# Kernel tuning notes

Measured on AMD Instinct MI355X. Metric: run time of the kernel, lower is better.

The kernel has to match this reference:

```python
import jax, jax.numpy as jnp
import numpy as np

IN_FEATURES = 512
OUT_FEATURES = 10
NEURONS_STRUCTURES = [64, 128, 256, 512]
REPETITIONS = 5
NUM_ACTIVATIONS = 4  # relu, tanh, sigmoid, gelu (exact erf, matching torch nn.GELU)
NUM_MODELS = NUM_ACTIVATIONS * REPETITIONS * len(NEURONS_STRUCTURES)  # 80
TOTAL_HIDDEN = sum(NEURONS_STRUCTURES) * REPETITIONS * NUM_ACTIVATIONS  # 19200
BATCH = 1024


def _build_neuron_model_id():
    # Mirrors ParallelMLPs.__init__ construction order:
    # for act -> for rep -> for structure: assign consecutive model ids
    ids = []
    m = 0
    for _act in range(NUM_ACTIVATIONS):
        for _rep in range(REPETITIONS):
            for n in NEURONS_STRUCTURES:
                ids += [m] * n
                m += 1
    return np.asarray(ids, dtype=np.int32)


def setup_inputs() -> dict:
    key = jax.random.key(0)
    k1, k2, k3, k4, k5 = jax.random.split(key, 5)
    x = jax.random.normal(k1, (BATCH, IN_FEATURES), dtype=jnp.float32)
    hidden_w = jax.random.normal(k2, (TOTAL_HIDDEN, IN_FEATURES), dtype=jnp.float32) * 0.05
    hidden_b = jax.random.normal(k3, (TOTAL_HIDDEN,), dtype=jnp.float32) * 0.05
    out_w = jax.random.normal(k4, (OUT_FEATURES, TOTAL_HIDDEN), dtype=jnp.float32) * 0.05
    out_b = jax.random.normal(k5, (NUM_MODELS, OUT_FEATURES), dtype=jnp.float32) * 0.05
    neuron_model_id = jnp.asarray(_build_neuron_model_id())
    return {"x": x, "hidden_w": hidden_w, "hidden_b": hidden_b,
            "out_w": out_w, "out_b": out_b, "neuron_model_id": neuron_model_id}


def reference(x, hidden_w, hidden_b, out_w, out_b, neuron_model_id):
    # Shared hidden linear: [B, H]
    h = x @ hidden_w.T + hidden_b
    # Per-block activations on equal contiguous chunks of the hidden dim
    split = TOTAL_HIDDEN // NUM_ACTIVATIONS
    acts = [jax.nn.relu, jnp.tanh, jax.nn.sigmoid,
            lambda t: jax.nn.gelu(t, approximate=False)]
    a = jnp.concatenate(
        [f(h[:, i * split:(i + 1) * split]) for i, f in enumerate(acts)], axis=1)
    # Ragged grouped out-projection: contrib[h, b, o] = a[b, h] * out_w[o, h]
    contrib = a.T[:, :, None] * out_w.T[:, None, :]  # [H, B, O]
    grouped = jax.ops.segment_sum(contrib, neuron_model_id,
                                  num_segments=NUM_MODELS)  # [M, B, O]
    return jnp.transpose(grouped, (1, 0, 2)) + out_b[None, :, :]  # [B, M, O]
```

## Files before the change

kernel.cpp:

```cpp
#include <hip/hip_runtime.h>
#include <hip/hip_bf16.h>
#include <cstdint>
#include <cstddef>


typedef unsigned short u16;
typedef unsigned int u32;
typedef __bf16 bf16x8 __attribute__((ext_vector_type(8)));
typedef float f32x4 __attribute__((ext_vector_type(4)));

__device__ __forceinline__ u16 f2bf(float f) {
  u32 u = __builtin_bit_cast(u32, f);
  u += 0x7fffu + ((u >> 16) & 1u);
  return (u16)(u >> 16);
}
__device__ __forceinline__ float bf2f(u16 s) {
  u32 u = ((u32)s) << 16;
  return __builtin_bit_cast(float, u);
}

__device__ __forceinline__ void async16(void* l, const void* g) {
  __builtin_amdgcn_global_load_lds(
      (__attribute__((address_space(1))) void*)(void*)g,
      (__attribute__((address_space(3))) void*)l, 16, 0, 0);
}

__global__ __launch_bounds__(256) void cvt_kernel(
    const float4* __restrict__ xs, uint2* __restrict__ xd, int nx4,
    const float4* __restrict__ ws, uint2* __restrict__ wd, int nw4) {
  int i = blockIdx.x * blockDim.x + threadIdx.x;
  if (i >= nx4 + nw4) return;
  const float4* s; uint2* d; int j;
  if (i < nx4) { s = xs; d = xd; j = i; }
  else         { s = ws; d = wd; j = i - nx4; }
  float4 f = s[j];
  uint2 o;
  o.x = (u32)f2bf(f.x) | ((u32)f2bf(f.y) << 16);
  o.y = (u32)f2bf(f.z) | ((u32)f2bf(f.w) << 16);
  d[j] = o;
}

__global__ __launch_bounds__(256, 2) void gemm_act_kernel(
    const u16* __restrict__ A,
    const u16* __restrict__ Bw,
    const float* __restrict__ hbias,
    u16* __restrict__ aout) {
  __shared__ char lds[65536];
  const int t = threadIdx.x;
  const int lane = t & 63;
  const int w = t >> 6;
  const int bx = blockIdx.x % 150;
  const int by = blockIdx.x / 150;
  const int row0 = by * 128;
  const int col0 = bx * 128;
  const int wr = w >> 1, wc = w & 1;

  f32x4 acc[4][4];
#pragma unroll
  for (int m = 0; m < 4; ++m)
#pragma unroll
    for (int n = 0; n < 4; ++n)
#pragma unroll
      for (int r = 0; r < 4; ++r) acc[m][n][r] = 0.f;

  const int srow = t >> 3;
  const int sc8 = t & 7;

  auto stage = [&](int buf, int kt) {
    const int k0 = kt * 64;
#pragma unroll
    for (int i = 0; i < 4; ++i) {
      int row = i * 32 + srow;
      int c8 = sc8 ^ (row & 7);
      const u16* gA = A + (size_t)(row0 + row) * 512 + k0 + c8 * 8;
      const u16* gB = Bw + (size_t)(col0 + row) * 512 + k0 + c8 * 8;
      char* lA = lds + buf * 16384 + i * 4096 + w * 1024;
      char* lB = lds + 32768 + buf * 16384 + i * 4096 + w * 1024;
      async16(lA, gA);
      async16(lB, gB);
    }
  };

  auto compute = [&](int buf) {
    const char* baseA = lds + buf * 16384;
    const char* baseB = lds + 32768 + buf * 16384;
    const int il = lane & 15;
    const int kb0 = (lane >> 4) * 16;
#pragma unroll
    for (int ks = 0; ks < 2; ++ks) {
      bf16x8 av[4], bv[4];
#pragma unroll
      for (int m = 0; m < 4; ++m) {
        int row = wr * 64 + m * 16 + il;
        int off = row * 128 + ((ks * 64 + kb0) ^ ((row & 7) << 4));
        av[m] = *(const bf16x8*)(baseA + off);
      }
#pragma unroll
      for (int n = 0; n < 4; ++n) {
        int row = wc * 64 + n * 16 + il;
        int off = row * 128 + ((ks * 64 + kb0) ^ ((row & 7) << 4));
        bv[n] = *(const bf16x8*)(baseB + off);
      }
#pragma unroll
      for (int m = 0; m < 4; ++m)
#pragma unroll
        for (int n = 0; n < 4; ++n)
          acc[m][n] = __builtin_amdgcn_mfma_f32_16x16x32_bf16(av[m], bv[n],
                                                              acc[m][n], 0, 0, 0);
    }
  };

  stage(0, 0);
  __syncthreads();
#pragma unroll 2
  for (int kt = 0; kt < 8; ++kt) {
    int cur = kt & 1;
    if (kt < 7) stage(cur ^ 1, kt + 1);
    compute(cur);
    __syncthreads();
  }

  const int il = lane & 15;
  const int q = lane >> 4;
#pragma unroll
  for (int n = 0; n < 4; ++n) {
    int gcol = col0 + wc * 64 + n * 16 + il;
    int act = gcol / 4800;
    float bias = hbias[gcol];
#pragma unroll
    for (int m = 0; m < 4; ++m) {
      int growb = row0 + wr * 64 + m * 16 + q * 4;
#pragma unroll
      for (int r = 0; r < 4; ++r) {
        float v = acc[m][n][r] + bias;
        float o;
        if (act == 0)      o = fmaxf(v, 0.f);
        else if (act == 1) o = tanhf(v);
        else if (act == 2) o = 1.f / (1.f + __expf(-v));
        else               o = 0.5f * v * (1.f + erff(v * 0.70710678118f));
        aout[(size_t)(growb + r) * 19200 + gcol] = f2bf(o);
      }
    }
  }
}

__global__ __launch_bounds__(256) void layer2_kernel(
    const u16* __restrict__ a,
    const float* __restrict__ ow,
    const float* __restrict__ ob,
    float* __restrict__ out) {
  const int t = threadIdx.x;
  const int wid = blockIdx.x * 4 + (t >> 6);
  const int lane = t & 63;
  const int m = wid >> 8;
  const int btile = wid & 255;
  const int g = lane >> 4;
  const int il = lane & 15;
  const int b = btile * 4 + g;
  const int s = m & 3;
  const int r5 = (m >> 2) % 5;
  const int act = m / 20;
  const int start = act * 4800 + r5 * 960 + 64 * ((1 << s) - 1);
  const int len = 64 << s;

  const u16* arow = a + (size_t)b * 19200 + start;
  float acc[10];
#pragma unroll
  for (int o = 0; o < 10; ++o) acc[o] = 0.f;

  for (int j = il; j < len; j += 16) {
    float av = bf2f(arow[j]);
    int col = start + j;
#pragma unroll
    for (int o = 0; o < 10; ++o)
      acc[o] = fmaf(av, ow[o * 19200 + col], acc[o]);
  }
#pragma unroll
  for (int o = 0; o < 10; ++o) {
    float v = acc[o];
    v += __shfl_xor(v, 1);
    v += __shfl_xor(v, 2);
    v += __shfl_xor(v, 4);
    v += __shfl_xor(v, 8);
    acc[o] = v;
  }
  if (il < 10) {
    float res = 0.f;
#pragma unroll
    for (int o = 0; o < 10; ++o)
      if (il == o) res = acc[o];
    out[(size_t)b * 800 + m * 10 + il] = res + ob[m * 10 + il];
  }
}

extern "C" void kernel_launch(void* const* d_in, const int* in_sizes, int n_in,
                              void* d_out, int out_size, void* d_ws, size_t ws_size,
                              hipStream_t stream) {
  const float* x = (const float*)d_in[0];
  const float* hw = (const float*)d_in[1];
  const float* hb = (const float*)d_in[2];
  const float* ow = (const float*)d_in[3];
  const float* ob = (const float*)d_in[4];
  float* out = (float*)d_out;

  char* ws = (char*)d_ws;
  u16* xb = (u16*)ws;
  u16* wb = (u16*)(ws + 1048576);
  u16* ab = (u16*)(ws + 1048576 + 19660800);

  const int nx4 = (1024 * 512) / 4;
  const int nw4 = (19200 * 512) / 4;
  const int tot = nx4 + nw4;
  cvt_kernel<<<tot / 256, 256, 0, stream>>>((const float4*)x, (uint2*)xb, nx4,
                                            (const float4*)hw, (uint2*)wb, nw4);
  gemm_act_kernel<<<1200, 256, 0, stream>>>(xb, wb, hb, ab);
  layer2_kernel<<<5120, 256, 0, stream>>>(ab, ow, ob, out);
}
```

Measured before the change: 181.5 us.

## Fuse out-projection into GEMM epilogue with atomic accumulation

Removes the bf16 activation buffer and the separate layer-2 kernel. The GEMM epilogue now multiplies the activated tile by out_w, reduces across lanes with shuffles and atomically adds into the output, which a new init kernel pre-fills with the output bias. The GEMM K-tile shrinks to 32 without swizzle and LDS use halves so three blocks can fit per CU, and the block order is reshaped so row tiles vary fastest. The cost is float atomics, a heavier epilogue with many shuffles, possible LDS bank conflicts from the unswizzled layout, and a summation order that is no longer deterministic.

New measurement: 302.5 us. 1.67x slower.

```diff
diff --git a/kernel.cpp b/kernel.cpp
--- a/kernel.cpp
+++ b/kernel.cpp
@@ -13,10 +13,6 @@
   u32 u = __builtin_bit_cast(u32, f);
   u += 0x7fffu + ((u >> 16) & 1u);
   return (u16)(u >> 16);
-}
-__device__ __forceinline__ float bf2f(u16 s) {
-  u32 u = ((u32)s) << 16;
-  return __builtin_bit_cast(float, u);
 }
 
 __device__ __forceinline__ void async16(void* l, const void* g) {
@@ -40,19 +36,25 @@
   d[j] = o;
 }
 
-__global__ __launch_bounds__(256, 2) void gemm_act_kernel(
+__global__ __launch_bounds__(256) void init_out_kernel(
+    const float* __restrict__ ob, float* __restrict__ out) {
+  int i = blockIdx.x * 256 + threadIdx.x;
+  out[i] = ob[i % 800];
+}
+
+__global__ __launch_bounds__(256, 3) void gemm_fused_kernel(
     const u16* __restrict__ A,
     const u16* __restrict__ Bw,
     const float* __restrict__ hbias,
-    u16* __restrict__ aout) {
-  __shared__ char lds[65536];
+    const float* __restrict__ ow,
+    float* __restrict__ out) {
+  __shared__ char lds[32768];
   const int t = threadIdx.x;
   const int lane = t & 63;
   const int w = t >> 6;
-  const int bx = blockIdx.x % 150;
-  const int by = blockIdx.x / 150;
-  const int row0 = by * 128;
-  const int col0 = bx * 128;
+  const int by = blockIdx.x & 7;
+  const int bx = blockIdx.x >> 3;
+  const int row0 = by * 128, col0 = bx * 128;
   const int wr = w >> 1, wc = w & 1;
 
   f32x4 acc[4][4];
@@ -63,133 +65,104 @@
 #pragma unroll
       for (int r = 0; r < 4; ++r) acc[m][n][r] = 0.f;
 
-  const int srow = t >> 3;
-  const int sc8 = t & 7;
+  const int srow = lane >> 2;
+  const int sk8 = lane & 3;
 
   auto stage = [&](int buf, int kt) {
-    const int k0 = kt * 64;
+    const int k0 = kt * 32 + sk8 * 8;
 #pragma unroll
-    for (int i = 0; i < 4; ++i) {
-      int row = i * 32 + srow;
-      int c8 = sc8 ^ (row & 7);
-      const u16* gA = A + (size_t)(row0 + row) * 512 + k0 + c8 * 8;
-      const u16* gB = Bw + (size_t)(col0 + row) * 512 + k0 + c8 * 8;
-      char* lA = lds + buf * 16384 + i * 4096 + w * 1024;
-      char* lB = lds + 32768 + buf * 16384 + i * 4096 + w * 1024;
-      async16(lA, gA);
-      async16(lB, gB);
+    for (int j = 0; j < 2; ++j) {
+      int row = j * 64 + w * 16 + srow;
+      async16(lds + buf * 8192 + j * 4096 + w * 1024,
+              A + (size_t)(row0 + row) * 512 + k0);
+      async16(lds + 16384 + buf * 8192 + j * 4096 + w * 1024,
+              Bw + (size_t)(col0 + row) * 512 + k0);
     }
   };
 
+  const int il = lane & 15, q = lane >> 4;
+
   auto compute = [&](int buf) {
-    const char* baseA = lds + buf * 16384;
-    const char* baseB = lds + 32768 + buf * 16384;
-    const int il = lane & 15;
-    const int kb0 = (lane >> 4) * 16;
+    const char* bA = lds + buf * 8192;
+    const char* bB = lds + 16384 + buf * 8192;
+    bf16x8 av[4], bv[4];
 #pragma unroll
-    for (int ks = 0; ks < 2; ++ks) {
-      bf16x8 av[4], bv[4];
+    for (int m = 0; m < 4; ++m)
+      av[m] = *(const bf16x8*)(bA + (wr * 64 + m * 16 + il) * 64 + q * 16);
 #pragma unroll
-      for (int m = 0; m < 4; ++m) {
-        int row = wr * 64 + m * 16 + il;
-        int off = row * 128 + ((ks * 64 + kb0) ^ ((row & 7) << 4));
-        av[m] = *(const bf16x8*)(baseA + off);
-      }
+    for (int n = 0; n < 4; ++n)
+      bv[n] = *(const bf16x8*)(bB + (wc * 64 + n * 16 + il) * 64 + q * 16);
 #pragma unroll
-      for (int n = 0; n < 4; ++n) {
-        int row = wc * 64 + n * 16 + il;
-        int off = row * 128 + ((ks * 64 + kb0) ^ ((row & 7) << 4));
-        bv[n] = *(const bf16x8*)(baseB + off);
-      }
+    for (int m = 0; m < 4; ++m)
 #pragma unroll
-      for (int m = 0; m < 4; ++m)
-#pragma unroll
-        for (int n = 0; n < 4; ++n)
-          acc[m][n] = __builtin_amdgcn_mfma_f32_16x16x32_bf16(av[m], bv[n],
-                                                              acc[m][n], 0, 0, 0);
-    }
+      for (int n = 0; n < 4; ++n)
+        acc[m][n] = __builtin_amdgcn_mfma_f32_16x16x32_bf16(av[m], bv[n],
+                                                            acc[m][n], 0, 0, 0);
   };
 
   stage(0, 0);
   __syncthreads();
-#pragma unroll 2
-  for (int kt = 0; kt < 8; ++kt) {
+  for (int kt = 0; kt < 16; ++kt) {
     int cur = kt & 1;
-    if (kt < 7) stage(cur ^ 1, kt + 1);
+    if (kt < 15) stage(cur ^ 1, kt + 1);
     compute(cur);
     __syncthreads();
   }
 
-  const int il = lane & 15;
-  const int q = lane >> 4;
+  const int colb = col0 + wc * 64;
+  const int actid = colb / 4800;
+  const int ch = colb % 4800;
+  const int rep = ch / 960, cc = ch % 960;
+  const int sid = cc < 64 ? 0 : cc < 192 ? 1 : cc < 448 ? 2 : 3;
+  const int m_id = actid * 20 + rep * 4 + sid;
+
+  int cols[4]; float bias[4];
 #pragma unroll
   for (int n = 0; n < 4; ++n) {
-    int gcol = col0 + wc * 64 + n * 16 + il;
-    int act = gcol / 4800;
-    float bias = hbias[gcol];
+    cols[n] = colb + n * 16 + il;
+    bias[n] = hbias[cols[n]];
+  }
+
 #pragma unroll
-    for (int m = 0; m < 4; ++m) {
-      int growb = row0 + wr * 64 + m * 16 + q * 4;
+  for (int m = 0; m < 4; ++m)
+#pragma unroll
+    for (int n = 0; n < 4; ++n)
 #pragma unroll
       for (int r = 0; r < 4; ++r) {
-        float v = acc[m][n][r] + bias;
+        float v = acc[m][n][r] + bias[n];
         float o;
-        if (act == 0)      o = fmaxf(v, 0.f);
-        else if (act == 1) o = tanhf(v);
-        else if (act == 2) o = 1.f / (1.f + __expf(-v));
-        else               o = 0.5f * v * (1.f + erff(v * 0.70710678118f));
-        aout[(size_t)(growb + r) * 19200 + gcol] = f2bf(o);
+        if (actid == 0)      o = fmaxf(v, 0.f);
+        else if (actid == 1) o = tanhf(v);
+        else if (actid == 2) o = 1.f / (1.f + __expf(-v));
+        else                 o = 0.5f * v * (1.f + erff(v * 0.70710678118f));
+        acc[m][n][r] = o;
       }
-    }
-  }
-}
 
-__global__ __launch_bounds__(256) void layer2_kernel(
-    const u16* __restrict__ a,
-    const float* __restrict__ ow,
-    const float* __restrict__ ob,
-    float* __restrict__ out) {
-  const int t = threadIdx.x;
-  const int wid = blockIdx.x * 4 + (t >> 6);
-  const int lane = t & 63;
-  const int m = wid >> 8;
-  const int btile = wid & 255;
-  const int g = lane >> 4;
-  const int il = lane & 15;
-  const int b = btile * 4 + g;
-  const int s = m & 3;
-  const int r5 = (m >> 2) % 5;
-  const int act = m / 20;
-  const int start = act * 4800 + r5 * 960 + 64 * ((1 << s) - 1);
-  const int len = 64 << s;
-
-  const u16* arow = a + (size_t)b * 19200 + start;
-  float acc[10];
-#pragma unroll
-  for (int o = 0; o < 10; ++o) acc[o] = 0.f;
-
-  for (int j = il; j < len; j += 16) {
-    float av = bf2f(arow[j]);
-    int col = start + j;
-#pragma unroll
-    for (int o = 0; o < 10; ++o)
-      acc[o] = fmaf(av, ow[o * 19200 + col], acc[o]);
-  }
+  const int obase = (row0 + wr * 64 + q * 4) * 800 + m_id * 10;
 #pragma unroll
   for (int o = 0; o < 10; ++o) {
-    float v = acc[o];
-    v += __shfl_xor(v, 1);
-    v += __shfl_xor(v, 2);
-    v += __shfl_xor(v, 4);
-    v += __shfl_xor(v, 8);
-    acc[o] = v;
-  }
-  if (il < 10) {
-    float res = 0.f;
+    float wv[4];
 #pragma unroll
-    for (int o = 0; o < 10; ++o)
-      if (il == o) res = acc[o];
-    out[(size_t)b * 800 + m * 10 + il] = res + ob[m * 10 + il];
+    for (int n = 0; n < 4; ++n) wv[n] = ow[o * 19200 + cols[n]];
+    float p[16];
+#pragma unroll
+    for (int m = 0; m < 4; ++m)
+#pragma unroll
+      for (int r = 0; r < 4; ++r)
+        p[m * 4 + r] = acc[m][0][r] * wv[0] + acc[m][1][r] * wv[1]
+                     + acc[m][2][r] * wv[2] + acc[m][3][r] * wv[3];
+#pragma unroll
+    for (int mask = 1; mask <= 8; mask <<= 1)
+#pragma unroll
+      for (int i = 0; i < 16; ++i)
+        p[i] += __shfl_xor(p[i], mask);
+    if (il == o) {
+#pragma unroll
+      for (int m = 0; m < 4; ++m)
+#pragma unroll
+        for (int r = 0; r < 4; ++r)
+          atomicAdd(&out[obase + m * 16 * 800 + r * 800 + o], p[m * 4 + r]);
+    }
   }
 }
 
@@ -206,13 +179,12 @@
   char* ws = (char*)d_ws;
   u16* xb = (u16*)ws;
   u16* wb = (u16*)(ws + 1048576);
-  u16* ab = (u16*)(ws + 1048576 + 19660800);
 
   const int nx4 = (1024 * 512) / 4;
   const int nw4 = (19200 * 512) / 4;
   const int tot = nx4 + nw4;
   cvt_kernel<<<tot / 256, 256, 0, stream>>>((const float4*)x, (uint2*)xb, nx4,
                                             (const float4*)hw, (uint2*)wb, nw4);
-  gemm_act_kernel<<<1200, 256, 0, stream>>>(xb, wb, hb, ab);
-  layer2_kernel<<<5120, 256, 0, stream>>>(ab, ow, ob, out);
+  init_out_kernel<<<3200, 256, 0, stream>>>(ob, out);
+  gemm_fused_kernel<<<1200, 256, 0, stream>>>(xb, wb, hb, ow, out);
 }
```
